# Performance work log

Measured on AMD Instinct MI355X. Metric: run time of the kernel, lower is better.

Reference implementation:

```python
import jax, jax.numpy as jnp
import numpy as np

NC = 80
REG = 16          # DFL bins per coordinate
CONF_THRES = 0.25
IOU_THRES = 0.45
MAX_DET = 300
TOPK = 1000       # fixed-size pre-NMS candidate pool (stand-in for max_nms=30000 with A=8400)
MAX_WH = 7680.0   # class offset for class-aware NMS
LEVELS = [(80, 80, 8.0), (40, 40, 16.0), (20, 20, 32.0)]  # (h, w, stride) for imgsz=640


def _make_anchors():
    """make_anchors: grid-cell centers (+0.5 offset) and per-anchor strides."""
    pts, strs = [], []
    for h, w, s in LEVELS:
        sx = jnp.arange(w, dtype=jnp.float32) + 0.5
        sy = jnp.arange(h, dtype=jnp.float32) + 0.5
        gy, gx = jnp.meshgrid(sy, sx, indexing='ij')
        pts.append(jnp.stack([gx, gy], -1).reshape(-1, 2))
        strs.append(jnp.full((h * w,), s, dtype=jnp.float32))
    return jnp.concatenate(pts).T, jnp.concatenate(strs)  # [2, A], [A]


def _box_iou(b):  # b: [K, 4] xyxy -> [K, K] pairwise IoU
    area = (b[:, 2] - b[:, 0]) * (b[:, 3] - b[:, 1])
    lt = jnp.maximum(b[:, None, :2], b[None, :, :2])
    rb = jnp.minimum(b[:, None, 2:], b[None, :, 2:])
    wh = jnp.clip(rb - lt, 0.0)
    inter = wh[..., 0] * wh[..., 1]
    return inter / (area[:, None] + area[None, :] - inter + 1e-7)


def _nms_keep(iou, valid):
    """Greedy NMS over score-sorted candidates: keep[i] iff valid and no earlier kept box overlaps > thr."""
    K = iou.shape[0]
    idx = jnp.arange(K)
    def body(keep, i):
        sup = jnp.any((iou[i] > IOU_THRES) & keep & (idx < i))
        return keep.at[i].set(valid[i] & jnp.logical_not(sup)), None
    keep, _ = jax.lax.scan(body, jnp.zeros(K, dtype=bool), idx)
    return keep


def _forward(preds, dfl_w):
    B, C, A = preds.shape
    # DFL decode: softmax over 16 bins, expectation with arange(16) weights (the 1x1 conv)
    box_logits = preds[:, :4 * REG].reshape(B, 4, REG, A)
    dist = jnp.einsum('bqra,r->bqa', jax.nn.softmax(box_logits, axis=2), dfl_w)  # [B,4,A] ltrb
    anc, strd = _make_anchors()
    lt, rb = dist[:, :2], dist[:, 2:]
    x1y1 = anc[None] - lt
    x2y2 = anc[None] + rb
    c_xy = (x1y1 + x2y2) / 2
    wh = x2y2 - x1y1
    dbox = jnp.concatenate([c_xy, wh], axis=1) * strd  # dist2bbox(xywh) * stride, [B,4,A]
    cls = jax.nn.sigmoid(preds[:, 4 * REG:])           # [B,NC,A]
    # xywh2xyxy
    cx, cy, w, h = dbox[:, 0], dbox[:, 1], dbox[:, 2], dbox[:, 3]
    boxes = jnp.stack([cx - w / 2, cy - h / 2, cx + w / 2, cy + h / 2], axis=-1)  # [B,A,4]
    conf = jnp.max(cls, axis=1)      # [B,A]
    j = jnp.argmax(cls, axis=1)      # [B,A]
    score = jnp.where(conf > CONF_THRES, conf, -1.0)
    top_s, top_i = jax.lax.top_k(score, TOPK)                               # [B,K]
    tb = jnp.take_along_axis(boxes, top_i[..., None], axis=1)               # [B,K,4]
    tj = jnp.take_along_axis(j, top_i, axis=1)                              # [B,K]
    valid = top_s > CONF_THRES
    ob = tb + (tj.astype(preds.dtype) * MAX_WH)[..., None]                  # class-offset boxes
    iou = jax.vmap(_box_iou)(ob)                                            # [B,K,K]
    keep = jax.vmap(_nms_keep)(iou, valid)                                  # [B,K]
    sel = jnp.where(keep, top_s, -1e9)
    order = jnp.argsort(-sel, axis=1)[:, :MAX_DET]                          # kept, score-sorted
    fb = jnp.take_along_axis(tb, order[..., None], axis=1)
    fs = jnp.take_along_axis(top_s, order, axis=1)
    fj = jnp.take_along_axis(tj, order, axis=1).astype(preds.dtype)
    fv = jnp.take_along_axis(keep, order, axis=1)
    out = jnp.concatenate([fb, fs[..., None], fj[..., None]], axis=-1)
    return out * fv[..., None].astype(preds.dtype)                          # [B,300,6]


def setup_inputs() -> dict:
    key = jax.random.key(0)
    k1, _ = jax.random.split(key)
    preds = jax.random.normal(k1, (32, 4 * REG + NC, 8400), dtype=jnp.float32)
    dfl_w = jnp.arange(REG, dtype=jnp.float32)
    return {"preds": preds, "dfl_w": dfl_w}


def reference(preds, dfl_w):
    return _forward(preds, dfl_w)
```

## Files before the change

### kernel.cpp

```cpp
#include <hip/hip_runtime.h>
#include <cstdint>
#include <cstddef>

typedef unsigned long long u64;
typedef unsigned int u32;

#define A_TOT   8400
#define NCLS    80
#define KSLOT   1024
#define NCHUNK  9
#define TOPK_N  1000
#define MAXDET  300
#define OUT_STRIDE (MAXDET * 6)

#define GLOBAL_AS const __attribute__((address_space(1))) void*
#define LDS_AS __attribute__((address_space(3))) void*


__device__ __forceinline__ float sig32(float x) {
#pragma clang fp contract(off)
    float e = (float)exp(-(double)x);
    float t = 1.0f + e;
    return 1.0f / t;
}

__device__ __forceinline__ u32 key_hi_from_score(float s) {
    u32 u = __float_as_uint(s);
    return (u & 0x80000000u) ? ~u : (u | 0x80000000u);
}
__device__ __forceinline__ float score_from_key_hi(u32 t) {
    u32 u = (t & 0x80000000u) ? (t ^ 0x80000000u) : ~t;
    return __uint_as_float(u);
}

__device__ __forceinline__ u64 mp_rank(const u64* A, const u64* B, int t) {
    int lo = 0, hi = t;
    while (lo < hi) {
        int mid = (lo + hi + 1) >> 1;
        if (A[mid - 1] > B[t - mid]) lo = mid; else hi = mid - 1;
    }
    int i = lo, j = t - lo;
    u64 av = A[i], bv = B[j];
    return av > bv ? av : bv;
}

__global__ __launch_bounds__(256) void k_decode(const float* __restrict__ preds,
                                                u64* __restrict__ key_raw,
                                                float4* __restrict__ dbox) {
#pragma clang fp contract(off)
    __shared__ float tile[2][16][256];
    int b = blockIdx.y;
    int a0 = blockIdx.x * 256;
    int t = threadIdx.x;
    int a = a0 + t;
    int nA = A_TOT - a0; if (nA > 256) nA = 256;
    int p4max = nA >> 2;
    const float* pb = preds + (size_t)b * 144 * A_TOT;

    int l  = t & 63;
    int wv = t >> 6;
    int lc = (l < p4max) ? l : (p4max - 1);

    auto stage = [&](int ch0, int buf) {
#pragma unroll
        for (int k = 0; k < 4; ++k) {
            int r = 4 * k + wv;
            const float* gsrc = pb + (size_t)(ch0 + r) * A_TOT + a0 + 4 * lc;
            __builtin_amdgcn_global_load_lds((GLOBAL_AS)gsrc,
                                             (LDS_AS)&tile[buf][r][0],
                                             16, 0, 0);
        }
    };

    float d[4] = {0.f, 0.f, 0.f, 0.f};
    float m = -3.0e38f, m2 = -3.0e38f;
    int jm = 0;

    stage(0, 0);
    __syncthreads();

    for (int cb = 0; cb < 9; ++cb) {
        int buf = cb & 1;
        if (cb + 1 < 9) stage((cb + 1) * 16, (cb + 1) & 1);
        if (t < nA) {
            float x[16];
#pragma unroll
            for (int r = 0; r < 16; ++r) x[r] = tile[buf][r][t];
            if (cb < 4) {
                float mx = x[0];
#pragma unroll
                for (int r = 1; r < 16; ++r) mx = fmaxf(mx, x[r]);
                float e[16], s = 0.f;
#pragma unroll
                for (int r = 0; r < 16; ++r) { e[r] = expf(x[r] - mx); s = s + e[r]; }
                float dd = 0.f;
#pragma unroll
                for (int r = 0; r < 16; ++r) { float pr = e[r] / s; dd = dd + pr * (float)r; }
                d[cb] = dd;
            } else {
                int cbase = (cb - 4) * 16;
#pragma unroll
                for (int r = 0; r < 16; ++r) {
                    int c = cbase + r;
                    float v = x[r];
                    if (v > m) { m2 = m; m = v; jm = c; }
                    else if (v > m2) { m2 = v; }
                }
            }
        }
        if (cb < 8) __syncthreads();
    }

    if (t >= nA) return;

    const float* pc = pb + (size_t)64 * A_TOT + a;
    float conf; int cls = jm;
    if ((m - m2) < 1e-4f || m > 7.0f) {
        float sb = -1.0f; int jb = 0;
        for (int c = 0; c < NCLS; ++c) {
            float s = sig32(pc[(size_t)c * A_TOT]);
            if (s > sb) { sb = s; jb = c; }
        }
        conf = sb; cls = jb;
    } else {
        conf = sig32(m);
    }
    float score = (conf > 0.25f) ? conf : -1.0f;
    u32 hi = key_hi_from_score(score);
    u32 lo = ((0x3FFFu - (u32)a) << 7) | (u32)cls;
    key_raw[(size_t)b * A_TOT + a] = ((u64)hi << 32) | lo;

    int row, col; float stride;
    if (a < 6400)      { row = a / 80;          col = a % 80;          stride = 8.0f; }
    else if (a < 8000) { int aa = a - 6400; row = aa / 40; col = aa % 40; stride = 16.0f; }
    else               { int aa = a - 8000; row = aa / 20; col = aa % 20; stride = 32.0f; }
    float ax = (float)col + 0.5f;
    float ay = (float)row + 0.5f;
    float x1 = ax - d[0], y1 = ay - d[1];
    float x2 = ax + d[2], y2 = ay + d[3];
    float cx = (x1 + x2) / 2.0f, cy = (y1 + y2) / 2.0f;
    float w  = x2 - x1,          h  = y2 - y1;
    float4 db;
    db.x = cx * stride; db.y = cy * stride; db.z = w * stride; db.w = h * stride;
    dbox[(size_t)b * A_TOT + a] = db;
}

__global__ __launch_bounds__(1024) void k_chunksort(const u64* __restrict__ key_raw,
                                                    u64* __restrict__ key_sorted) {
    __shared__ u64 s[KSLOT];
    int b = blockIdx.y, ch = blockIdx.x, t = threadIdx.x;
    int a = ch * KSLOT + t;
    s[t] = (a < A_TOT) ? key_raw[(size_t)b * A_TOT + a] : 0ull;
    __syncthreads();
    for (int k = 2; k <= KSLOT; k <<= 1) {
        for (int j = k >> 1; j > 0; j >>= 1) {
            int ixj = t ^ j;
            if (ixj > t) {
                u64 x = s[t], y = s[ixj];
                bool descBlock = ((t & k) == 0);
                bool sw = descBlock ? (x < y) : (x > y);
                if (sw) { s[t] = y; s[ixj] = x; }
            }
            __syncthreads();
        }
    }
    key_sorted[((size_t)b * NCHUNK + ch) * KSLOT + t] = s[t];
}

__global__ __launch_bounds__(1024) void k_select(const u64* __restrict__ key_sorted,
                                                 u64* __restrict__ topk,
                                                 const float4* __restrict__ dbox,
                                                 float* __restrict__ tb,
                                                 float* __restrict__ ob,
                                                 float* __restrict__ area,
                                                 u32* __restrict__ validf) {
#pragma clang fp contract(off)
    __shared__ u64 L[5 * KSLOT];
    int b = blockIdx.x, t = threadIdx.x;
    const u64* KS = key_sorted + (size_t)b * NCHUNK * KSLOT;

    u64 r0 = mp_rank(KS + 0 * KSLOT, KS + 1 * KSLOT, t);
    u64 r1 = mp_rank(KS + 2 * KSLOT, KS + 3 * KSLOT, t);
    u64 r2 = mp_rank(KS + 4 * KSLOT, KS + 5 * KSLOT, t);
    u64 r3 = mp_rank(KS + 6 * KSLOT, KS + 7 * KSLOT, t);
    u64 r4 = KS[8 * KSLOT + t];
    L[0 * KSLOT + t] = r0; L[1 * KSLOT + t] = r1;
    L[2 * KSLOT + t] = r2; L[3 * KSLOT + t] = r3;
    L[4 * KSLOT + t] = r4;
    __syncthreads();

    u64 m0 = mp_rank(L + 0 * KSLOT, L + 1 * KSLOT, t);
    u64 m1 = mp_rank(L + 2 * KSLOT, L + 3 * KSLOT, t);
    __syncthreads();
    L[0 * KSLOT + t] = m0; L[1 * KSLOT + t] = m1;
    __syncthreads();

    u64 s0 = mp_rank(L + 0 * KSLOT, L + 1 * KSLOT, t);
    __syncthreads();
    L[0 * KSLOT + t] = s0;
    __syncthreads();

    u64 key = mp_rank(L + 0 * KSLOT, L + 4 * KSLOT, t);
    size_t si = (size_t)b * KSLOT + t;
    topk[si] = key;

    u32 hi = (u32)(key >> 32);
    u32 lo = (u32)key;
    bool valid = (t < TOPK_N) && (hi & 0x80000000u);
    if (!valid) {
        tb[si*4+0]=0.f; tb[si*4+1]=0.f; tb[si*4+2]=0.f; tb[si*4+3]=0.f;
        ob[si*4+0]=0.f; ob[si*4+1]=0.f; ob[si*4+2]=0.f; ob[si*4+3]=0.f;
        area[si] = 0.f; validf[si] = 0u;
        return;
    }
    int a   = 0x3FFF - (int)((lo >> 7) & 0x3FFFu);
    int cls = (int)(lo & 0x7Fu);

    float4 db = dbox[(size_t)b * A_TOT + a];
    float bx1 = db.x - db.z / 2.0f, by1 = db.y - db.w / 2.0f;
    float bx2 = db.x + db.z / 2.0f, by2 = db.y + db.w / 2.0f;
    tb[si*4+0] = bx1; tb[si*4+1] = by1; tb[si*4+2] = bx2; tb[si*4+3] = by2;

    float off = (float)cls * 7680.0f;
    float o0 = bx1 + off, o1 = by1 + off, o2 = bx2 + off, o3 = by2 + off;
    ob[si*4+0] = o0; ob[si*4+1] = o1; ob[si*4+2] = o2; ob[si*4+3] = o3;
    area[si] = (o2 - o0) * (o3 - o1);
    validf[si] = 1u;
}

__global__ __launch_bounds__(256) void k_matrix(const float* __restrict__ ob,
                                                const float* __restrict__ area,
                                                u64* __restrict__ masks) {
#pragma clang fp contract(off)
    __shared__ float4 sob[KSLOT];
    __shared__ float  sar[KSLOT];
    int b = blockIdx.y, rblk = blockIdx.x, tid = threadIdx.x;
    const float4* gob = (const float4*)(ob + (size_t)b * KSLOT * 4);
    const float*  gar = area + (size_t)b * KSLOT;
    for (int i = tid; i < KSLOT; i += blockDim.x) { sob[i] = gob[i]; sar[i] = gar[i]; }
    __syncthreads();

    int lane = tid & 63;
    int wave = tid >> 6;
    int i = rblk * 64 + lane;
    float4 bi = sob[i];
    float Ai = sar[i];

#pragma unroll
    for (int wl = 0; wl < 4; ++wl) {
        int w = wave * 4 + wl;
        u64 mword = 0ull;
        if (w >= rblk) {
            for (int bit = 0; bit < 64; ++bit) {
                int j = (w << 6) + bit;
                float4 bj = sob[j];
                float Aj = sar[j];
                float lt0 = fmaxf(bi.x, bj.x);
                float lt1 = fmaxf(bi.y, bj.y);
                float rb0 = fminf(bi.z, bj.z);
                float rb1 = fminf(bi.w, bj.w);
                float ww = fmaxf(rb0 - lt0, 0.0f);
                float hh = fmaxf(rb1 - lt1, 0.0f);
                float inter = ww * hh;
                float den = ((Ai + Aj) - inter) + 1e-7f;
                float iou = inter / den;
                if ((j > i) && (iou > 0.45f)) mword |= (1ull << bit);
            }
        }
        masks[((size_t)b * KSLOT + i) * 16 + w] = mword;
    }
}

__global__ __launch_bounds__(64) void k_scan(const u64* __restrict__ masks,
                                             const u32* __restrict__ validf,
                                             u64* __restrict__ keep) {
    __shared__ u64 rows[KSLOT];
    int b = blockIdx.x, lane = threadIdx.x;
    const char* base = (const char*)(masks + (size_t)b * KSLOT * 16);

    float4 r0, r1, r2, r3, r4, r5, r6, r7;
    {
        const float4* src = (const float4*)base;
        r0 = src[0*64 + lane]; r1 = src[1*64 + lane];
        r2 = src[2*64 + lane]; r3 = src[3*64 + lane];
        r4 = src[4*64 + lane]; r5 = src[5*64 + lane];
        r6 = src[6*64 + lane]; r7 = src[7*64 + lane];
    }

    u64 kw = 0ull;
    u64 rem = 0ull;
    int kept = 0;

    for (int w = 0; w < 16; ++w) {
        {
            float4* dst = (float4*)rows;
            dst[0*64 + lane] = r0; dst[1*64 + lane] = r1;
            dst[2*64 + lane] = r2; dst[3*64 + lane] = r3;
            dst[4*64 + lane] = r4; dst[5*64 + lane] = r5;
            dst[6*64 + lane] = r6; dst[7*64 + lane] = r7;
        }
        u32 vf = validf[(size_t)b * KSLOT + w * 64 + lane];
        u64 valid_w = __ballot(vf != 0u);
        __syncthreads();
        if (w < 15) {
            const float4* src = (const float4*)(base + (size_t)(w + 1) * 8192);
            r0 = src[0*64 + lane]; r1 = src[1*64 + lane];
            r2 = src[2*64 + lane]; r3 = src[3*64 + lane];
            r4 = src[4*64 + lane]; r5 = src[5*64 + lane];
            r6 = src[6*64 + lane]; r7 = src[7*64 + lane];
        }

        u64 live = valid_w & ~__shfl(rem, w);
        while (live) {
            int i = __ffsll(live) - 1;
            if (lane == w) kw |= (1ull << i);
            u64 m = (lane < 16) ? rows[i * 16 + lane] : 0ull;
            rem |= m;
            ++kept;
            if (kept >= MAXDET) break;
            live &= ~(__shfl(m, w) | (1ull << i));
        }
        if (kept >= MAXDET) break;
        __syncthreads();
    }
    if (lane < 16) keep[(size_t)b * 16 + lane] = kw;
}

__global__ __launch_bounds__(1024) void k_final(const u64* __restrict__ keep,
                                                const u64* __restrict__ topk,
                                                const float* __restrict__ tb,
                                                float* __restrict__ out) {
    __shared__ u64 kw[16];
    __shared__ int pref[16];
    int b = blockIdx.x, t = threadIdx.x;
    float* ob_ = out + (size_t)b * OUT_STRIDE;
    for (int i = t; i < OUT_STRIDE; i += blockDim.x) ob_[i] = 0.0f;
    if (t < 16) kw[t] = keep[(size_t)b * 16 + t];
    __syncthreads();
    if (t == 0) {
        int s = 0;
        for (int w = 0; w < 16; ++w) { pref[w] = s; s += __popcll(kw[w]); }
    }
    __syncthreads();
    int w = t >> 6, bit = t & 63;
    bool kp = (kw[w] >> bit) & 1ull;
    if (kp) {
        u64 below = (bit == 0) ? 0ull : (kw[w] & ((1ull << bit) - 1ull));
        int rank = pref[w] + __popcll(below);
        if (rank < MAXDET) {
            size_t si = (size_t)b * KSLOT + t;
            u64 key = topk[si];
            u32 hi = (u32)(key >> 32);
            u32 lo = (u32)key;
            float score = score_from_key_hi(hi);
            float clsf = (float)(lo & 0x7Fu);
            float* o = ob_ + rank * 6;
            o[0] = tb[si*4+0]; o[1] = tb[si*4+1];
            o[2] = tb[si*4+2]; o[3] = tb[si*4+3];
            o[4] = score; o[5] = clsf;
        }
    }
}

extern "C" void kernel_launch(void* const* d_in, const int* in_sizes, int n_in,
                              void* d_out, int out_size, void* d_ws, size_t ws_size,
                              hipStream_t stream) {
    const float* preds = (const float*)d_in[0];
    float* out = (float*)d_out;
    int B = in_sizes[0] / (144 * A_TOT);

    char* ws = (char*)d_ws;
    size_t off = 0;
    u64* key_raw    = (u64*)(ws + off); off += (size_t)B * A_TOT * 8;
    u64* key_sorted = (u64*)(ws + off); off += (size_t)B * NCHUNK * KSLOT * 8;
    u64* topk       = (u64*)(ws + off); off += (size_t)B * KSLOT * 8;
    float4* dbox    = (float4*)(ws + off); off += (size_t)B * A_TOT * 16;
    float* tb       = (float*)(ws + off); off += (size_t)B * KSLOT * 4 * 4;
    float* obuf     = (float*)(ws + off); off += (size_t)B * KSLOT * 4 * 4;
    float* area     = (float*)(ws + off); off += (size_t)B * KSLOT * 4;
    u32* validf     = (u32*)(ws + off); off += (size_t)B * KSLOT * 4;
    u64* masks      = (u64*)(ws + off); off += (size_t)B * KSLOT * 16 * 8;
    u64* keep       = (u64*)(ws + off); off += (size_t)B * 16 * 8;

    k_decode<<<dim3((A_TOT + 255) / 256, B), 256, 0, stream>>>(preds, key_raw, dbox);
    k_chunksort<<<dim3(NCHUNK, B), KSLOT, 0, stream>>>(key_raw, key_sorted);
    k_select<<<B, KSLOT, 0, stream>>>(key_sorted, topk, dbox, tb, obuf, area, validf);
    k_matrix<<<dim3(16, B), 256, 0, stream>>>(obuf, area, masks);
    k_scan<<<B, 64, 0, stream>>>(masks, validf, keep);
    k_final<<<B, 1024, 0, stream>>>(keep, topk, tb, out);
}
```

Measured before the change: 166.4 us.

## Restructure NMS scan: register-held self-word, padded LDS rows, deferred suppression OR

Reworks the serial greedy NMS scan kernel. Each lane now holds its own row's intra-chunk mask word in a register, so the serial loop resolves suppression with one shuffle per kept box and no LDS read. The OR into the remaining-suppression mask is deferred until after the chunk finishes. Valid-flag ballots are hoisted out of the loop, and the LDS rows are padded to 17 words to avoid bank conflicts. The intent is to shorten the latency-bound dependency chain of the serial loop, at the cost of a second pass over kept rows per chunk.

```diff
diff --git a/kernel.cpp b/kernel.cpp
--- a/kernel.cpp
+++ b/kernel.cpp
@@ -274,56 +274,71 @@
 __global__ __launch_bounds__(64) void k_scan(const u64* __restrict__ masks,
                                              const u32* __restrict__ validf,
                                              u64* __restrict__ keep) {
-    __shared__ u64 rows[KSLOT];
+    __shared__ u64 rows[64][17];
     int b = blockIdx.x, lane = threadIdx.x;
-    const char* base = (const char*)(masks + (size_t)b * KSLOT * 16);
-
-    float4 r0, r1, r2, r3, r4, r5, r6, r7;
-    {
-        const float4* src = (const float4*)base;
-        r0 = src[0*64 + lane]; r1 = src[1*64 + lane];
-        r2 = src[2*64 + lane]; r3 = src[3*64 + lane];
-        r4 = src[4*64 + lane]; r5 = src[5*64 + lane];
-        r6 = src[6*64 + lane]; r7 = src[7*64 + lane];
-    }
-
-    u64 kw = 0ull;
+    const ulonglong2* base = (const ulonglong2*)(masks + (size_t)b * KSLOT * 16);
+
+    u32 vf[16];
+#pragma unroll
+    for (int w = 0; w < 16; ++w)
+        vf[w] = validf[(size_t)b * KSLOT + w * 64 + lane];
+    u64 vws[16];
+#pragma unroll
+    for (int w = 0; w < 16; ++w)
+        vws[w] = __ballot(vf[w] != 0u);
+
+    ulonglong2 r0 = base[0*64 + lane], r1 = base[1*64 + lane];
+    ulonglong2 r2 = base[2*64 + lane], r3 = base[3*64 + lane];
+    ulonglong2 r4 = base[4*64 + lane], r5 = base[5*64 + lane];
+    ulonglong2 r6 = base[6*64 + lane], r7 = base[7*64 + lane];
+
+    int srow = lane >> 3;
+    int sw0  = (lane & 7) * 2;
+
+    u64 my_kw = 0ull;
     u64 rem = 0ull;
     int kept = 0;
 
     for (int w = 0; w < 16; ++w) {
-        {
-            float4* dst = (float4*)rows;
-            dst[0*64 + lane] = r0; dst[1*64 + lane] = r1;
-            dst[2*64 + lane] = r2; dst[3*64 + lane] = r3;
-            dst[4*64 + lane] = r4; dst[5*64 + lane] = r5;
-            dst[6*64 + lane] = r6; dst[7*64 + lane] = r7;
-        }
-        u32 vf = validf[(size_t)b * KSLOT + w * 64 + lane];
-        u64 valid_w = __ballot(vf != 0u);
+        rows[0*8+srow][sw0] = r0.x; rows[0*8+srow][sw0+1] = r0.y;
+        rows[1*8+srow][sw0] = r1.x; rows[1*8+srow][sw0+1] = r1.y;
+        rows[2*8+srow][sw0] = r2.x; rows[2*8+srow][sw0+1] = r2.y;
+        rows[3*8+srow][sw0] = r3.x; rows[3*8+srow][sw0+1] = r3.y;
+        rows[4*8+srow][sw0] = r4.x; rows[4*8+srow][sw0+1] = r4.y;
+        rows[5*8+srow][sw0] = r5.x; rows[5*8+srow][sw0+1] = r5.y;
+        rows[6*8+srow][sw0] = r6.x; rows[6*8+srow][sw0+1] = r6.y;
+        rows[7*8+srow][sw0] = r7.x; rows[7*8+srow][sw0+1] = r7.y;
         __syncthreads();
         if (w < 15) {
-            const float4* src = (const float4*)(base + (size_t)(w + 1) * 8192);
+            const ulonglong2* src = base + (size_t)(w + 1) * 512;
             r0 = src[0*64 + lane]; r1 = src[1*64 + lane];
             r2 = src[2*64 + lane]; r3 = src[3*64 + lane];
             r4 = src[4*64 + lane]; r5 = src[5*64 + lane];
             r6 = src[6*64 + lane]; r7 = src[7*64 + lane];
         }
 
-        u64 live = valid_w & ~__shfl(rem, w);
+        u64 S = rows[lane][w];
+        u64 live = vws[w] & ~__shfl(rem, w);
+        u64 keep_w = 0ull;
         while (live) {
             int i = __ffsll(live) - 1;
-            if (lane == w) kw |= (1ull << i);
-            u64 m = (lane < 16) ? rows[i * 16 + lane] : 0ull;
-            rem |= m;
+            keep_w |= (1ull << i);
             ++kept;
             if (kept >= MAXDET) break;
-            live &= ~(__shfl(m, w) | (1ull << i));
-        }
+            live &= ~(__shfl(S, i) | (1ull << i));
+        }
+        if (lane == w) my_kw = keep_w;
         if (kept >= MAXDET) break;
+        if (w < 15) {
+            u64 kk = keep_w;
+            while (kk) {
+                int i = __ffsll(kk) - 1; kk &= kk - 1;
+                rem |= (lane < 16) ? rows[i][lane] : 0ull;
+            }
+        }
         __syncthreads();
     }
-    if (lane < 16) keep[(size_t)b * 16 + lane] = kw;
+    if (lane < 16) keep[(size_t)b * 16 + lane] = my_kw;
 }
 
 __global__ __launch_bounds__(1024) void k_final(const u64* __restrict__ keep,
```

Measured after the change: 175.8 us. +5.6%, slower.
